# Performance work log

Measured on AMD Instinct MI355X. Metric: run time of the kernel, lower is better.

## Reference

```python
import jax, jax.numpy as jnp
import numpy as np
import math

WH, WW = 7, 7          # window size
N = WH * WW            # tokens per window = 49
H = 12                 # num heads
C = 384                # dim
D = C // H             # head dim = 32
NW = 64                # num windows (56x56 map, 7x7 windows)
B = 32                 # image batch
BW = B * NW            # windowed batch = 2048


def _cpb_constants():
    # log-spaced continuous relative coords table, flattened to [(2*WH-1)*(2*WW-1), 2]
    rh = np.arange(-(WH - 1), WH, dtype=np.float32)
    rw = np.arange(-(WW - 1), WW, dtype=np.float32)
    t = np.stack(np.meshgrid(rh, rw, indexing='ij'), axis=-1)  # [13,13,2]
    t[..., 0] /= (WH - 1)
    t[..., 1] /= (WW - 1)
    t *= 8.0
    t = np.sign(t) * np.log2(np.abs(t) + 1.0) / np.log2(8.0)
    # relative position index [N*N]
    ch, cw = np.meshgrid(np.arange(WH), np.arange(WW), indexing='ij')
    cf = np.stack([ch.ravel(), cw.ravel()])            # [2, N]
    rel = cf[:, :, None] - cf[:, None, :]              # [2, N, N]
    rel = rel.transpose(1, 2, 0).astype(np.int64)      # [N, N, 2]
    rel[..., 0] += WH - 1
    rel[..., 1] += WW - 1
    rel[..., 0] *= 2 * WW - 1
    rpi = rel.sum(-1).reshape(-1)                      # [N*N]
    return jnp.asarray(t.reshape(-1, 2)), jnp.asarray(rpi)

_COORDS_TABLE, _RPI = _cpb_constants()


def setup_inputs() -> dict:
    key = jax.random.key(0)
    ks = jax.random.split(key, 8)
    x = jax.random.normal(ks[0], (BW, N, C), dtype=jnp.float32)
    # shifted-window style 0/-100 mask
    mask = jnp.where(jax.random.uniform(ks[1], (NW, N, N)) < 0.1, -100.0, 0.0).astype(jnp.float32)
    qkv_w = jax.random.normal(ks[2], (3 * C, C), dtype=jnp.float32) * 0.02
    q_bias = jnp.zeros((C,), dtype=jnp.float32)
    v_bias = jnp.zeros((C,), dtype=jnp.float32)
    logit_scale = jnp.full((H, 1, 1), math.log(10.0), dtype=jnp.float32)
    cpb_w1 = jax.random.normal(ks[3], (512, 2), dtype=jnp.float32) * 0.02
    cpb_b1 = jnp.zeros((512,), dtype=jnp.float32)
    cpb_w2 = jax.random.normal(ks[4], (H, 512), dtype=jnp.float32) * 0.02
    proj_w = jax.random.normal(ks[5], (C, C), dtype=jnp.float32) * 0.02
    proj_b = jnp.zeros((C,), dtype=jnp.float32)
    return {"x": x, "mask": mask, "qkv_w": qkv_w, "q_bias": q_bias, "v_bias": v_bias,
            "logit_scale": logit_scale, "cpb_w1": cpb_w1, "cpb_b1": cpb_b1,
            "cpb_w2": cpb_w2, "proj_w": proj_w, "proj_b": proj_b}


def reference(x, mask, qkv_w, q_bias, v_bias, logit_scale, cpb_w1, cpb_b1, cpb_w2, proj_w, proj_b):
    B_, n, c = x.shape
    # qkv projection; k has no bias (registered zeros buffer)
    qkv_bias = jnp.concatenate([q_bias, jnp.zeros_like(q_bias), v_bias])
    qkv = x @ qkv_w.T + qkv_bias                              # [B_, N, 3C]
    qkv = qkv.reshape(B_, n, 3, H, D).transpose(2, 0, 3, 1, 4)  # [3, B_, H, N, D]
    q, k, v = qkv[0], qkv[1], qkv[2]
    # cosine attention
    qn = q / jnp.clip(jnp.linalg.norm(q, axis=-1, keepdims=True), 1e-12)
    kn = k / jnp.clip(jnp.linalg.norm(k, axis=-1, keepdims=True), 1e-12)
    attn = jnp.einsum('bhnd,bhmd->bhnm', qn, kn)              # [B_, H, N, N]
    scale = jnp.exp(jnp.minimum(logit_scale, math.log(1.0 / 0.01)))  # [H,1,1]
    attn = attn * scale
    # continuous position bias MLP + gather
    hid = jax.nn.relu(_COORDS_TABLE @ cpb_w1.T + cpb_b1)      # [169, 512]
    bias_tab = hid @ cpb_w2.T                                  # [169, H]
    rpb = bias_tab[_RPI].reshape(n, n, H).transpose(2, 0, 1)  # [H, N, N]
    rpb = 16.0 * jax.nn.sigmoid(rpb)
    attn = attn + rpb[None]
    # shifted-window mask add
    nW = mask.shape[0]
    attn = attn.reshape(B_ // nW, nW, H, n, n) + mask[None, :, None]
    attn = jax.nn.softmax(attn.reshape(B_, H, n, n), axis=-1)
    out = jnp.einsum('bhnm,bhmd->bnhd', attn, v).reshape(B_, n, c)
    return out @ proj_w.T + proj_b
```

## Files before the change

kernel.cpp:

```cpp
#include <hip/hip_runtime.h>
#include <hip/hip_bf16.h>
#include <math.h>

#define NTOK 49
#define NH 12
#define HD 32
#define CDIM 384
#define NWIN 64
#define BWIN 2048
#define QKVROW 1152
#define BCROW 52
#define BCTILE 2560

typedef __bf16 bf16x8 __attribute__((ext_vector_type(8)));
typedef __bf16 bf16x4 __attribute__((ext_vector_type(4)));
typedef float f32x4 __attribute__((ext_vector_type(4)));

__device__ __forceinline__ void gload_lds16(const void* g, void* l) {
    __builtin_amdgcn_global_load_lds((const __attribute__((address_space(1))) void*)g,
                                     (__attribute__((address_space(3))) void*)l, 16, 0, 0);
}

__device__ __forceinline__ void cvt8(const float* src, __bf16* dst, int i) {
    f32x4 a = *(const f32x4*)(src + (size_t)i * 8);
    f32x4 b = *(const f32x4*)(src + (size_t)i * 8 + 4);
    bf16x8 o;
#pragma unroll
    for (int e = 0; e < 4; ++e) { o[e] = (__bf16)a[e]; o[e + 4] = (__bf16)b[e]; }
    *(bf16x8*)(dst + (size_t)i * 8) = o;
}

#define XBLKS 18816
__global__ void prep1(const float* __restrict__ x, __bf16* __restrict__ xbf,
                      const float* __restrict__ qkv_w, __bf16* __restrict__ qkv_wb,
                      const float* __restrict__ proj_w, __bf16* __restrict__ proj_wb,
                      const float* __restrict__ w1, const float* __restrict__ b1,
                      const float* __restrict__ w2, float* __restrict__ bias_tab) {
    const int blk = blockIdx.x, tid = threadIdx.x;
    if (blk < XBLKS) {
        cvt8(x, xbf, blk * 256 + tid);
    } else if (blk < XBLKS + 216) {
        cvt8(qkv_w, qkv_wb, (blk - XBLKS) * 256 + tid);
    } else if (blk < XBLKS + 288) {
        cvt8(proj_w, proj_wb, (blk - XBLKS - 216) * 256 + tid);
    } else {
        int t = (blk - XBLKS - 288) * 256 + tid;
        if (t >= 169 * NH) return;
        int r = t / NH, h = t - (t / NH) * NH;
        int i = r / 13, j = r - (r / 13) * 13;
        float a0 = (float)(i - 6) * (8.0f / 6.0f);
        float a1 = (float)(j - 6) * (8.0f / 6.0f);
        float c0 = copysignf(log2f(fabsf(a0) + 1.0f) * (1.0f / 3.0f), a0);
        float c1 = copysignf(log2f(fabsf(a1) + 1.0f) * (1.0f / 3.0f), a1);
        float sum = 0.f;
        for (int k = 0; k < 512; ++k) {
            float hid = c0 * w1[2 * k] + c1 * w1[2 * k + 1] + b1[k];
            hid = fmaxf(hid, 0.f);
            sum += hid * w2[h * 512 + k];
        }
        bias_tab[r * NH + h] = sum;
    }
}

__global__ void prep2(const float* __restrict__ bias_tab, const float* __restrict__ mask,
                      float* __restrict__ biasC) {
    int idx = blockIdx.x * blockDim.x + threadIdx.x;
    if (idx >= NWIN * NH * NTOK * BCROW) return;
    const int per_t = NTOK * BCROW;
    int wh = idx / per_t;
    int rem = idx - wh * per_t;
    int q = rem / BCROW, k = rem - (rem / BCROW) * BCROW;
    int w = wh / NH, h = wh - (wh / NH) * NH;
    float* dst = biasC + (size_t)wh * BCTILE + q * BCROW + k;
    if (k < NTOK) {
        int chi = q / 7, cwi = q - (q / 7) * 7;
        int chj = k / 7, cwj = k - (k / 7) * 7;
        int rpi = (chi - chj + 6) * 13 + (cwi - cwj + 6);
        float r = bias_tab[rpi * NH + h];
        *dst = 16.f / (1.f + __expf(-r)) + mask[(w * NTOK + q) * NTOK + k];
    } else {
        *dst = 0.f;
    }
}

template <int MODE, int NBY>
__global__ __launch_bounds__(256) void gemm6(
    const __bf16* __restrict__ A, const __bf16* __restrict__ Bw,
    const float* __restrict__ qbias, const float* __restrict__ vbias,
    __bf16* __restrict__ qkvout,
    float* __restrict__ fout, const float* __restrict__ fbias)
{
    __shared__ __bf16 As[3][128 * 32];
    __shared__ __bf16 Bs[3][128 * 32];
    const int tid = threadIdx.x;
    const int chunk = (784 * NBY) >> 3;
    const int wg = (blockIdx.x & 7) * chunk + (blockIdx.x >> 3);
    const int gx = wg / NBY, gy = wg - (wg / NBY) * NBY;
    const int lane = tid & 63;
    const int wid = tid >> 6;
    const int wr = (wid >> 1) * 64;
    const int wc = (wid & 1) * 64;
    const int fr = lane & 15;
    const int fq = lane >> 4;

    f32x4 acc[4][4];
#pragma unroll
    for (int m = 0; m < 4; ++m)
#pragma unroll
        for (int n = 0; n < 4; ++n)
            acc[m][n] = (f32x4){0.f, 0.f, 0.f, 0.f};

    const int srow0 = tid >> 2, scp0 = tid & 3;
    const int srow1 = (256 + tid) >> 2;
    const size_t ar0 = (size_t)(gx * 128 + srow0) * CDIM + (scp0 ^ ((srow0 >> 1) & 3)) * 8;
    const size_t ar1 = (size_t)(gx * 128 + srow1) * CDIM + (scp0 ^ ((srow1 >> 1) & 3)) * 8;
    const size_t br0 = (size_t)(gy * 128 + srow0) * CDIM + (scp0 ^ ((srow0 >> 1) & 3)) * 8;
    const size_t br1 = (size_t)(gy * 128 + srow1) * CDIM + (scp0 ^ ((srow1 >> 1) & 3)) * 8;
    const int ls0 = tid * 16, ls1 = (256 + tid) * 16;

#define STAGE(ti, buf) do {                                              \
        const int kk_ = (ti) * 32;                                       \
        gload_lds16(A + ar0 + kk_, (char*)&As[buf][0] + ls0);            \
        gload_lds16(A + ar1 + kk_, (char*)&As[buf][0] + ls1);            \
        gload_lds16(Bw + br0 + kk_, (char*)&Bs[buf][0] + ls0);           \
        gload_lds16(Bw + br1 + kk_, (char*)&Bs[buf][0] + ls1);           \
    } while (0)

    STAGE(0, 0);
    STAGE(1, 1);

#pragma unroll
    for (int t = 0; t < 12; ++t) {
        if (t < 11) asm volatile("s_waitcnt vmcnt(4)" ::: "memory");
        else        asm volatile("s_waitcnt vmcnt(0)" ::: "memory");
        __builtin_amdgcn_s_barrier();
        if (t + 2 < 12) STAGE(t + 2, (t + 2) % 3);
        const int cur = t % 3;
        bf16x8 af[4], bfr[4];
#pragma unroll
        for (int m = 0; m < 4; ++m) {
            const int row = wr + m * 16 + fr;
            af[m] = *(const bf16x8*)&As[cur][row * 32 + (fq ^ ((row >> 1) & 3)) * 8];
        }
#pragma unroll
        for (int n = 0; n < 4; ++n) {
            const int row = wc + n * 16 + fr;
            bfr[n] = *(const bf16x8*)&Bs[cur][row * 32 + (fq ^ ((row >> 1) & 3)) * 8];
        }
#pragma unroll
        for (int m = 0; m < 4; ++m)
#pragma unroll
            for (int n = 0; n < 4; ++n)
                acc[m][n] = __builtin_amdgcn_mfma_f32_16x16x32_bf16(af[m], bfr[n], acc[m][n], 0, 0, 0);
    }
#undef STAGE

    if (MODE == 0) {
        const int colbase = gy * 128;
        const int part = colbase / CDIM;
        const int pcolbase = colbase - part * CDIM;
#pragma unroll
        for (int m = 0; m < 4; ++m) {
#pragma unroll
            for (int r = 0; r < 4; ++r) {
                const int row = gx * 128 + wr + m * 16 + fq * 4 + r;
                __bf16* orow = qkvout + (size_t)row * QKVROW + colbase + wc;
#pragma unroll
                for (int n = 0; n < 4; ++n) {
                    const int pcol = pcolbase + wc + n * 16 + fr;
                    float val = acc[m][n][r];
                    if (part == 0) val += qbias[pcol];
                    if (part == 2) val += vbias[pcol];
                    orow[n * 16 + fr] = (__bf16)val;
                }
            }
        }
    } else {
#pragma unroll
        for (int m = 0; m < 4; ++m) {
#pragma unroll
            for (int r = 0; r < 4; ++r) {
                const int row = gx * 128 + wr + m * 16 + fq * 4 + r;
                float* orow = fout + (size_t)row * CDIM + gy * 128 + wc;
#pragma unroll
                for (int n = 0; n < 4; ++n) {
                    const int col = gy * 128 + wc + n * 16 + fr;
                    orow[n * 16 + fr] = acc[m][n][r] + fbias[col];
                }
            }
        }
    }
}

#define WREG 15872
__global__ __launch_bounds__(256) void attn2(
    const __bf16* __restrict__ qkv, const float* __restrict__ biasC,
    const float* __restrict__ lscale, __bf16* __restrict__ aout)
{
    __shared__ char smem[4 * WREG];
    const int tid = threadIdx.x;
    const int wid = tid >> 6, lane = tid & 63;
    const int bh = blockIdx.x * 4 + wid;
    const int b = bh / NH, h = bh - b * NH;
    const int w = b & (NWIN - 1);
    const int c = lane & 15, g = lane >> 4;

    char* base = smem + wid * WREG;
    __bf16* Kl = (__bf16*)base;
    __bf16* Ql = (__bf16*)(base + 5120);
    __bf16* Vl = (__bf16*)(base + 10240);
    float* invq = (float*)(base + 15360);
    float* invk = (float*)(base + 15616);
    char* Pl = base;

    const float sc = __expf(fminf(lscale[h], 4.6051702f));

    {
        const int row = lane;
        const size_t rb = ((size_t)b * NTOK + row) * QKVROW + h * HD;
        bf16x8 z;
#pragma unroll
        for (int e = 0; e < 8; ++e) z[e] = (__bf16)0.f;
        {
            bf16x8 t[4];
            float ss = 0.f;
            if (row < NTOK) {
#pragma unroll
                for (int ch = 0; ch < 4; ++ch) {
                    t[ch] = *(const bf16x8*)(qkv + rb + ch * 8);
#pragma unroll
                    for (int e = 0; e < 8; ++e) { float f = (float)t[ch][e]; ss += f * f; }
                }
            } else {
#pragma unroll
                for (int ch = 0; ch < 4; ++ch) t[ch] = z;
            }
#pragma unroll
            for (int ch = 0; ch < 4; ++ch) *(bf16x8*)&Ql[row * 40 + ch * 8] = t[ch];
            invq[row] = sc / fmaxf(sqrtf(ss), 1e-12f);
        }
        {
            bf16x8 t[4];
            float ss = 0.f;
            if (row < NTOK) {
#pragma unroll
                for (int ch = 0; ch < 4; ++ch) {
                    t[ch] = *(const bf16x8*)(qkv + rb + CDIM + ch * 8);
#pragma unroll
                    for (int e = 0; e < 8; ++e) { float f = (float)t[ch][e]; ss += f * f; }
                }
            } else {
#pragma unroll
                for (int ch = 0; ch < 4; ++ch) t[ch] = z;
            }
#pragma unroll
            for (int ch = 0; ch < 4; ++ch) *(bf16x8*)&Kl[row * 40 + ch * 8] = t[ch];
            invk[row] = 1.f / fmaxf(sqrtf(ss), 1e-12f);
        }
        {
            bf16x8 t[4];
            if (row < NTOK) {
#pragma unroll
                for (int ch = 0; ch < 4; ++ch) t[ch] = *(const bf16x8*)(qkv + rb + 2 * CDIM + ch * 8);
            } else {
#pragma unroll
                for (int ch = 0; ch < 4; ++ch) t[ch] = z;
            }
#pragma unroll
            for (int ch = 0; ch < 4; ++ch) *(bf16x8*)&Vl[row * 40 + ch * 8] = t[ch];
        }
    }

    bf16x8 kfr[4], qfr[4];
#pragma unroll
    for (int mt = 0; mt < 4; ++mt) kfr[mt] = *(const bf16x8*)&Kl[(mt * 16 + c) * 40 + g * 8];
#pragma unroll
    for (int nt = 0; nt < 4; ++nt) qfr[nt] = *(const bf16x8*)&Ql[(nt * 16 + c) * 40 + g * 8];
    f32x4 S[4][4];
#pragma unroll
    for (int mt = 0; mt < 4; ++mt)
#pragma unroll
        for (int nt = 0; nt < 4; ++nt) {
            S[mt][nt] = (f32x4){0.f, 0.f, 0.f, 0.f};
            S[mt][nt] = __builtin_amdgcn_mfma_f32_16x16x32_bf16(kfr[mt], qfr[nt], S[mt][nt], 0, 0, 0);
        }

    const float* bc = biasC + (size_t)(w * NH + h) * BCTILE;
    float ivq[4];
#pragma unroll
    for (int nt = 0; nt < 4; ++nt) ivq[nt] = invq[nt * 16 + c];
#pragma unroll
    for (int mt = 0; mt < 4; ++mt) {
        const int k0 = mt * 16 + g * 4;
#pragma unroll
        for (int nt = 0; nt < 4; ++nt) {
            const int q = nt * 16 + c;
            f32x4 bv = (f32x4){0.f, 0.f, 0.f, 0.f};
            if (q < NTOK) bv = *(const f32x4*)(bc + q * BCROW + k0);
#pragma unroll
            for (int r = 0; r < 4; ++r) {
                const int k = k0 + r;
                float v = S[mt][nt][r] * invk[k] * ivq[nt];
                if (k < NTOK) {
                    if (q < NTOK) v += bv[r];
                } else {
                    v = -1e30f;
                }
                S[mt][nt][r] = v;
            }
        }
    }

    float rs[4];
#pragma unroll
    for (int nt = 0; nt < 4; ++nt) {
        float m = -1e30f;
#pragma unroll
        for (int mt = 0; mt < 4; ++mt)
#pragma unroll
            for (int r = 0; r < 4; ++r) m = fmaxf(m, S[mt][nt][r]);
        m = fmaxf(m, __shfl_xor(m, 16));
        m = fmaxf(m, __shfl_xor(m, 32));
        float s = 0.f;
#pragma unroll
        for (int mt = 0; mt < 4; ++mt)
#pragma unroll
            for (int r = 0; r < 4; ++r) {
                float e = __expf(S[mt][nt][r] - m);
                S[mt][nt][r] = e;
                s += e;
            }
        s += __shfl_xor(s, 16);
        s += __shfl_xor(s, 32);
        rs[nt] = 1.f / s;
    }

#pragma unroll
    for (int mt = 0; mt < 4; ++mt)
#pragma unroll
        for (int nt = 0; nt < 4; ++nt) {
            bf16x4 pk;
#pragma unroll
            for (int r = 0; r < 4; ++r) pk[r] = (__bf16)(S[mt][nt][r] * rs[nt]);
            *(bf16x4*)(Pl + (nt * 16 + c) * 144 + (mt * 16 + g * 4) * 2) = pk;
        }

    bf16x8 vfr[2][2];
#pragma unroll
    for (int kt = 0; kt < 2; ++kt)
#pragma unroll
        for (int dt = 0; dt < 2; ++dt) {
            bf16x8 t;
#pragma unroll
            for (int e = 0; e < 8; ++e) t[e] = Vl[(kt * 32 + g * 8 + e) * 40 + dt * 16 + c];
            vfr[kt][dt] = t;
        }
    f32x4 O[4][2];
#pragma unroll
    for (int mt = 0; mt < 4; ++mt)
#pragma unroll
        for (int dt = 0; dt < 2; ++dt) O[mt][dt] = (f32x4){0.f, 0.f, 0.f, 0.f};
#pragma unroll
    for (int mt = 0; mt < 4; ++mt)
#pragma unroll
        for (int kt = 0; kt < 2; ++kt) {
            bf16x8 pfr = *(const bf16x8*)(Pl + (mt * 16 + c) * 144 + kt * 64 + g * 16);
#pragma unroll
            for (int dt = 0; dt < 2; ++dt)
                O[mt][dt] = __builtin_amdgcn_mfma_f32_16x16x32_bf16(pfr, vfr[kt][dt], O[mt][dt], 0, 0, 0);
        }

#pragma unroll
    for (int mt = 0; mt < 4; ++mt)
#pragma unroll
        for (int r = 0; r < 4; ++r) {
            const int q = mt * 16 + g * 4 + r;
            if (q < NTOK) {
                const size_t off = ((size_t)b * NTOK + q) * CDIM + h * HD;
                aout[off + c] = (__bf16)O[mt][0][r];
                aout[off + 16 + c] = (__bf16)O[mt][1][r];
            }
        }
}

extern "C" void kernel_launch(void* const* d_in, const int* in_sizes, int n_in,
                              void* d_out, int out_size, void* d_ws, size_t ws_size,
                              hipStream_t stream) {
    const float* x      = (const float*)d_in[0];
    const float* mask   = (const float*)d_in[1];
    const float* qkv_w  = (const float*)d_in[2];
    const float* q_bias = (const float*)d_in[3];
    const float* v_bias = (const float*)d_in[4];
    const float* lscale = (const float*)d_in[5];
    const float* cpb_w1 = (const float*)d_in[6];
    const float* cpb_b1 = (const float*)d_in[7];
    const float* cpb_w2 = (const float*)d_in[8];
    const float* proj_w = (const float*)d_in[9];
    const float* proj_b = (const float*)d_in[10];
    float* out = (float*)d_out;

    const size_t NROWS = (size_t)BWIN * NTOK;
    __bf16* qkvbuf  = (__bf16*)d_ws;
    __bf16* xbf     = qkvbuf + NROWS * QKVROW;
    __bf16* aoutbuf = xbf;
    __bf16* qkv_wb  = xbf + NROWS * CDIM;
    __bf16* proj_wb = qkv_wb + QKVROW * CDIM;
    float*  bias_tab = (float*)(proj_wb + CDIM * CDIM);
    float*  biasC   = bias_tab + 169 * NH;

    hipLaunchKernelGGL(prep1, dim3(XBLKS + 296), dim3(256), 0, stream,
                       x, xbf, qkv_w, qkv_wb, proj_w, proj_wb,
                       cpb_w1, cpb_b1, cpb_w2, bias_tab);
    hipLaunchKernelGGL(prep2, dim3((NWIN * NH * NTOK * BCROW + 255) / 256), dim3(256), 0, stream,
                       bias_tab, mask, biasC);
    hipLaunchKernelGGL((gemm6<0, 9>), dim3(784 * 9), dim3(256), 0, stream,
                       xbf, qkv_wb, q_bias, v_bias, qkvbuf, (float*)nullptr,
                       (const float*)nullptr);
    hipLaunchKernelGGL(attn2, dim3(BWIN * NH / 4), dim3(256), 0, stream,
                       qkvbuf, biasC, lscale, aoutbuf);
    hipLaunchKernelGGL((gemm6<1, 3>), dim3(784 * 3), dim3(256), 0, stream,
                       aoutbuf, proj_wb, (const float*)nullptr, (const float*)nullptr,
                       (__bf16*)nullptr, out, proj_b);
}
```

Before: 421.3 us.

## Shrink attention LDS footprint by reusing one buffer for K, Q and P

The attention kernel now stages K, then Q, then the probability tile in the same per-wave LDS region, processing P·V in two key halves so the P buffer is 80-byte rows instead of 144. The per-wave region drops from 15872 to 10496 bytes, so more blocks can be resident per CU. The Q norm is computed in registers and broadcast with shuffles instead of through LDS, and the inverse K norms are read as a vector. The cost is more sequential reuse of one buffer within each wave, which lengthens its dependency chain.

```diff
diff --git a/kernel.cpp b/kernel.cpp
--- a/kernel.cpp
+++ b/kernel.cpp
@@ -192,12 +192,12 @@
     }
 }
 
-#define WREG 15872
-__global__ __launch_bounds__(256) void attn2(
+#define AWREG 10496
+__global__ __launch_bounds__(256) void attn6(
     const __bf16* __restrict__ qkv, const float* __restrict__ biasC,
     const float* __restrict__ lscale, __bf16* __restrict__ aout)
 {
-    __shared__ char smem[4 * WREG];
+    __shared__ char smem[4 * AWREG];
     const int tid = threadIdx.x;
     const int wid = tid >> 6, lane = tid & 63;
     const int bh = blockIdx.x * 4 + wid;
@@ -205,77 +205,83 @@
     const int w = b & (NWIN - 1);
     const int c = lane & 15, g = lane >> 4;
 
-    char* base = smem + wid * WREG;
-    __bf16* Kl = (__bf16*)base;
-    __bf16* Ql = (__bf16*)(base + 5120);
-    __bf16* Vl = (__bf16*)(base + 10240);
-    float* invq = (float*)(base + 15360);
-    float* invk = (float*)(base + 15616);
-    char* Pl = base;
+    char* base = smem + wid * AWREG;
+    __bf16* Bn = (__bf16*)base;
+    __bf16* Vl = (__bf16*)(base + 5120);
+    float* invk = (float*)(base + 10240);
 
     const float sc = __expf(fminf(lscale[h], 4.6051702f));
 
+    bf16x8 z;
+#pragma unroll
+    for (int e = 0; e < 8; ++e) z[e] = (__bf16)0.f;
+
+    const int row = lane;
+    const size_t rb = ((size_t)b * NTOK + row) * QKVROW + h * HD;
+
     {
-        const int row = lane;
-        const size_t rb = ((size_t)b * NTOK + row) * QKVROW + h * HD;
-        bf16x8 z;
-#pragma unroll
-        for (int e = 0; e < 8; ++e) z[e] = (__bf16)0.f;
-        {
-            bf16x8 t[4];
-            float ss = 0.f;
-            if (row < NTOK) {
-#pragma unroll
-                for (int ch = 0; ch < 4; ++ch) {
-                    t[ch] = *(const bf16x8*)(qkv + rb + ch * 8);
-#pragma unroll
-                    for (int e = 0; e < 8; ++e) { float f = (float)t[ch][e]; ss += f * f; }
-                }
-            } else {
-#pragma unroll
-                for (int ch = 0; ch < 4; ++ch) t[ch] = z;
-            }
-#pragma unroll
-            for (int ch = 0; ch < 4; ++ch) *(bf16x8*)&Ql[row * 40 + ch * 8] = t[ch];
-            invq[row] = sc / fmaxf(sqrtf(ss), 1e-12f);
-        }
-        {
-            bf16x8 t[4];
-            float ss = 0.f;
-            if (row < NTOK) {
-#pragma unroll
-                for (int ch = 0; ch < 4; ++ch) {
-                    t[ch] = *(const bf16x8*)(qkv + rb + CDIM + ch * 8);
-#pragma unroll
-                    for (int e = 0; e < 8; ++e) { float f = (float)t[ch][e]; ss += f * f; }
-                }
-            } else {
-#pragma unroll
-                for (int ch = 0; ch < 4; ++ch) t[ch] = z;
-            }
-#pragma unroll
-            for (int ch = 0; ch < 4; ++ch) *(bf16x8*)&Kl[row * 40 + ch * 8] = t[ch];
-            invk[row] = 1.f / fmaxf(sqrtf(ss), 1e-12f);
-        }
-        {
-            bf16x8 t[4];
-            if (row < NTOK) {
-#pragma unroll
-                for (int ch = 0; ch < 4; ++ch) t[ch] = *(const bf16x8*)(qkv + rb + 2 * CDIM + ch * 8);
-            } else {
-#pragma unroll
-                for (int ch = 0; ch < 4; ++ch) t[ch] = z;
-            }
-#pragma unroll
-            for (int ch = 0; ch < 4; ++ch) *(bf16x8*)&Vl[row * 40 + ch * 8] = t[ch];
-        }
-    }
-
-    bf16x8 kfr[4], qfr[4];
-#pragma unroll
-    for (int mt = 0; mt < 4; ++mt) kfr[mt] = *(const bf16x8*)&Kl[(mt * 16 + c) * 40 + g * 8];
-#pragma unroll
-    for (int nt = 0; nt < 4; ++nt) qfr[nt] = *(const bf16x8*)&Ql[(nt * 16 + c) * 40 + g * 8];
+        bf16x8 t[4];
+        if (row < NTOK) {
+#pragma unroll
+            for (int ch = 0; ch < 4; ++ch) t[ch] = *(const bf16x8*)(qkv + rb + 2 * CDIM + ch * 8);
+        } else {
+#pragma unroll
+            for (int ch = 0; ch < 4; ++ch) t[ch] = z;
+        }
+#pragma unroll
+        for (int ch = 0; ch < 4; ++ch) *(bf16x8*)&Vl[row * 40 + ch * 8] = t[ch];
+    }
+
+    {
+        bf16x8 t[4];
+        float ss = 0.f;
+        if (row < NTOK) {
+#pragma unroll
+            for (int ch = 0; ch < 4; ++ch) {
+                t[ch] = *(const bf16x8*)(qkv + rb + CDIM + ch * 8);
+#pragma unroll
+                for (int e = 0; e < 8; ++e) { float f = (float)t[ch][e]; ss += f * f; }
+            }
+        } else {
+#pragma unroll
+            for (int ch = 0; ch < 4; ++ch) t[ch] = z;
+        }
+#pragma unroll
+        for (int ch = 0; ch < 4; ++ch) *(bf16x8*)&Bn[row * 40 + ch * 8] = t[ch];
+        invk[row] = 1.f / fmaxf(sqrtf(ss), 1e-12f);
+    }
+
+    bf16x8 kfr[4];
+#pragma unroll
+    for (int mt = 0; mt < 4; ++mt) kfr[mt] = *(const bf16x8*)&Bn[(mt * 16 + c) * 40 + g * 8];
+
+    float ssq = 0.f;
+    {
+        bf16x8 t[4];
+        if (row < NTOK) {
+#pragma unroll
+            for (int ch = 0; ch < 4; ++ch) {
+                t[ch] = *(const bf16x8*)(qkv + rb + ch * 8);
+#pragma unroll
+                for (int e = 0; e < 8; ++e) { float f = (float)t[ch][e]; ssq += f * f; }
+            }
+        } else {
+#pragma unroll
+            for (int ch = 0; ch < 4; ++ch) t[ch] = z;
+        }
+#pragma unroll
+        for (int ch = 0; ch < 4; ++ch) *(bf16x8*)&Bn[row * 40 + ch * 8] = t[ch];
+    }
+
+    bf16x8 qfr[4];
+    float ivq[4];
+#pragma unroll
+    for (int nt = 0; nt < 4; ++nt) {
+        qfr[nt] = *(const bf16x8*)&Bn[(nt * 16 + c) * 40 + g * 8];
+        float ss = __shfl(ssq, nt * 16 + c);
+        ivq[nt] = sc / fmaxf(sqrtf(ss), 1e-12f);
+    }
+
     f32x4 S[4][4];
 #pragma unroll
     for (int mt = 0; mt < 4; ++mt)
@@ -286,12 +292,10 @@
         }
 
     const float* bc = biasC + (size_t)(w * NH + h) * BCTILE;
-    float ivq[4];
-#pragma unroll
-    for (int nt = 0; nt < 4; ++nt) ivq[nt] = invq[nt * 16 + c];
 #pragma unroll
     for (int mt = 0; mt < 4; ++mt) {
         const int k0 = mt * 16 + g * 4;
+        const f32x4 ivkv = *(const f32x4*)&invk[k0];
 #pragma unroll
         for (int nt = 0; nt < 4; ++nt) {
             const int q = nt * 16 + c;
@@ -300,7 +304,7 @@
 #pragma unroll
             for (int r = 0; r < 4; ++r) {
                 const int k = k0 + r;
-                float v = S[mt][nt][r] * invk[k] * ivq[nt];
+                float v = S[mt][nt][r] * ivkv[r] * ivq[nt];
                 if (k < NTOK) {
                     if (q < NTOK) v += bv[r];
                 } else {
@@ -335,40 +339,41 @@
         rs[nt] = 1.f / s;
     }
 
+    f32x4 O[4][2];
 #pragma unroll
     for (int mt = 0; mt < 4; ++mt)
 #pragma unroll
-        for (int nt = 0; nt < 4; ++nt) {
-            bf16x4 pk;
-#pragma unroll
-            for (int r = 0; r < 4; ++r) pk[r] = (__bf16)(S[mt][nt][r] * rs[nt]);
-            *(bf16x4*)(Pl + (nt * 16 + c) * 144 + (mt * 16 + g * 4) * 2) = pk;
-        }
-
-    bf16x8 vfr[2][2];
-#pragma unroll
-    for (int kt = 0; kt < 2; ++kt)
+        for (int dt = 0; dt < 2; ++dt) O[mt][dt] = (f32x4){0.f, 0.f, 0.f, 0.f};
+
+#pragma unroll
+    for (int kt = 0; kt < 2; ++kt) {
+#pragma unroll
+        for (int mtl = 0; mtl < 2; ++mtl) {
+            const int mt = kt * 2 + mtl;
+#pragma unroll
+            for (int nt = 0; nt < 4; ++nt) {
+                bf16x4 pk;
+#pragma unroll
+                for (int r = 0; r < 4; ++r) pk[r] = (__bf16)(S[mt][nt][r] * rs[nt]);
+                *(bf16x4*)((char*)Bn + (nt * 16 + c) * 80 + (mtl * 16 + g * 4) * 2) = pk;
+            }
+        }
+        bf16x8 vfr[2];
 #pragma unroll
         for (int dt = 0; dt < 2; ++dt) {
             bf16x8 t;
 #pragma unroll
             for (int e = 0; e < 8; ++e) t[e] = Vl[(kt * 32 + g * 8 + e) * 40 + dt * 16 + c];
-            vfr[kt][dt] = t;
-        }
-    f32x4 O[4][2];
-#pragma unroll
-    for (int mt = 0; mt < 4; ++mt)
-#pragma unroll
-        for (int dt = 0; dt < 2; ++dt) O[mt][dt] = (f32x4){0.f, 0.f, 0.f, 0.f};
-#pragma unroll
-    for (int mt = 0; mt < 4; ++mt)
-#pragma unroll
-        for (int kt = 0; kt < 2; ++kt) {
-            bf16x8 pfr = *(const bf16x8*)(Pl + (mt * 16 + c) * 144 + kt * 64 + g * 16);
+            vfr[dt] = t;
+        }
+#pragma unroll
+        for (int mtO = 0; mtO < 4; ++mtO) {
+            bf16x8 pfr = *(const bf16x8*)((char*)Bn + (mtO * 16 + c) * 80 + g * 16);
 #pragma unroll
             for (int dt = 0; dt < 2; ++dt)
-                O[mt][dt] = __builtin_amdgcn_mfma_f32_16x16x32_bf16(pfr, vfr[kt][dt], O[mt][dt], 0, 0, 0);
-        }
+                O[mtO][dt] = __builtin_amdgcn_mfma_f32_16x16x32_bf16(pfr, vfr[dt], O[mtO][dt], 0, 0, 0);
+        }
+    }
 
 #pragma unroll
     for (int mt = 0; mt < 4; ++mt)
@@ -416,7 +421,7 @@
     hipLaunchKernelGGL((gemm6<0, 9>), dim3(784 * 9), dim3(256), 0, stream,
                        xbf, qkv_wb, q_bias, v_bias, qkvbuf, (float*)nullptr,
                        (const float*)nullptr);
-    hipLaunchKernelGGL(attn2, dim3(BWIN * NH / 4), dim3(256), 0, stream,
+    hipLaunchKernelGGL(attn6, dim3(BWIN * NH / 4), dim3(256), 0, stream,
                        qkvbuf, biasC, lscale, aoutbuf);
     hipLaunchKernelGGL((gemm6<1, 3>), dim3(784 * 3), dim3(256), 0, stream,
                        aoutbuf, proj_wb, (const float*)nullptr, (const float*)nullptr,
```

Measured after the change: 423.4 us. Within noise of the previous version (+0.5%).
